# Optimization experiments

Hardware: AMD Instinct MI355X
Metric: run time of the kernel (lower is better)

Reference implementation:

```python
import jax, jax.numpy as jnp
import numpy as np
import math

D_MODEL = 768
N_HEAD = 12
HEAD_DIM = D_MODEL // N_HEAD
B = 4
W = 32
HW = W * W


def setup_inputs() -> dict:
    key = jax.random.key(0)
    k1, k2, k3 = jax.random.split(key, 3)
    x = jax.random.normal(k1, (B, HW, D_MODEL), dtype=jnp.float32)
    w_qkv = jax.random.normal(k2, (3 * D_MODEL, D_MODEL), dtype=jnp.float32) * (D_MODEL ** -0.5)
    w_out = jax.random.normal(k3, (D_MODEL, D_MODEL), dtype=jnp.float32) * (D_MODEL ** -0.5)
    gamma = jnp.ones((D_MODEL,), dtype=jnp.float32)
    return {"x": x, "w_qkv": w_qkv, "w_out": w_out, "gamma": gamma}


def _axial_sincos(w, head_dim, dtype):
    # Axial RoPE: first half of head_dim encodes row position, second half column.
    dim_half = head_dim // 2
    inv_freq = 1.0 / (10000.0 ** (jnp.arange(0, dim_half, 2, dtype=dtype) / dim_half))  # (dim_half//2,)
    pos = jnp.arange(w, dtype=dtype)
    ang = pos[:, None] * inv_freq[None, :]                 # (w, f)
    row = jnp.repeat(ang[:, None, :], w, axis=1)           # (w, w, f)
    col = jnp.repeat(ang[None, :, :], w, axis=0)           # (w, w, f)
    theta = jnp.concatenate([row, col], axis=-1).reshape(w * w, dim_half)  # (hw, head_dim//2)
    theta = jnp.concatenate([theta, theta], axis=-1)       # rotate-half layout -> (hw, head_dim)
    return jnp.sin(theta), jnp.cos(theta)


def _rotate_half(t):
    t1, t2 = jnp.split(t, 2, axis=-1)
    return jnp.concatenate([-t2, t1], axis=-1)


def _apply_rotary(t, sin, cos):
    return t * cos + _rotate_half(t) * sin


def _rms_norm(x, gamma, eps=1e-6):
    return x * jax.lax.rsqrt(jnp.mean(x * x, axis=-1, keepdims=True) + eps) * gamma


def _attn_mask(w):
    # Faithful to the torch source: mask[center, neighbor] = False, else True.
    # torch SDPA bool semantics: True = attend. So 3x3 neighbors are EXCLUDED.
    idx = jnp.arange(w * w)
    r, c = idx // w, idx % w
    neighbor = (jnp.abs(r[:, None] - r[None, :]) <= 1) & (jnp.abs(c[:, None] - c[None, :]) <= 1)
    return ~neighbor  # (hw, hw) bool, True = allowed


def reference(x, w_qkv, w_out, gamma):
    Bx, hw, d = x.shape
    w = int(math.isqrt(hw))
    h, hd = N_HEAD, HEAD_DIM
    sin, cos = _axial_sincos(w, hd, x.dtype)               # (hw, hd) each
    xn = _rms_norm(x, gamma)
    qkv = xn @ w_qkv.T                                     # (B, hw, 3d)
    qkv = qkv.reshape(Bx, hw, 3, h, hd)
    q = jnp.transpose(qkv[:, :, 0], (0, 2, 1, 3))          # (B, h, hw, hd)
    k = jnp.transpose(qkv[:, :, 1], (0, 2, 1, 3))
    v = jnp.transpose(qkv[:, :, 2], (0, 2, 1, 3))
    q = _apply_rotary(q, sin, cos)
    k = _apply_rotary(k, sin, cos)
    allow = _attn_mask(w)
    scale = 1.0 / jnp.sqrt(jnp.asarray(hd, x.dtype))
    scores = jnp.einsum('bhid,bhjd->bhij', q, k) * scale   # (B, h, hw, hw)
    scores = jnp.where(allow[None, None], scores, jnp.asarray(-jnp.inf, x.dtype))
    probs = jax.nn.softmax(scores, axis=-1)
    out = jnp.einsum('bhij,bhjd->bhid', probs, v)          # (B, h, hw, hd)
    out = jnp.transpose(out, (0, 2, 1, 3)).reshape(Bx, hw, d)
    return out @ w_out.T
```

## Files before the change

kernel.cpp:

```cpp
#include <hip/hip_runtime.h>

typedef __attribute__((ext_vector_type(8))) short short8;
typedef __attribute__((ext_vector_type(4))) float f32x4;
typedef __attribute__((ext_vector_type(4))) unsigned short ushort4_t;
typedef unsigned short ushort_t;
typedef unsigned long long u64;

#define D_MODEL 768
#define NHEAD 12
#define HD 64
#define BATCH 4
#define HWIDTH 32
#define HW 1024
#define TOK (BATCH*HW)
#define QKV_N (3*D_MODEL)
#define BH (BATCH*NHEAD)
#define QSCALE 0.18033688f

__device__ __forceinline__ ushort_t f2bf(float f) {
    union { float f; unsigned u; } v; v.f = f;
    unsigned u = v.u;
    unsigned r = u + 0x7FFFu + ((u >> 16) & 1u);
    return (ushort_t)(r >> 16);
}
__device__ __forceinline__ float ex2(float x) {
    float r; asm("v_exp_f32 %0, %1" : "=v"(r) : "v"(x)); return r;
}
__device__ __forceinline__ unsigned cvtpk(float lo, float hi) {
    unsigned r; asm("v_cvt_pk_bf16_f32 %0, %1, %2" : "=v"(r) : "v"(lo), "v"(hi)); return r;
}

__global__ __launch_bounds__(256) void prep_kernel(const float* __restrict__ x,
                                                   const float* __restrict__ gamma,
                                                   ushort_t* __restrict__ xn,
                                                   const float* __restrict__ w_qkv,
                                                   ushort_t* __restrict__ wq,
                                                   const float* __restrict__ w_out,
                                                   ushort_t* __restrict__ wo,
                                                   float* __restrict__ sint,
                                                   float* __restrict__ cost) {
    int blk = blockIdx.x;
    if (blk < 1024) {
        int wave = threadIdx.x >> 6, lane = threadIdx.x & 63;
        int t = blk * 4 + wave;
        const float* xr = x + (size_t)t * D_MODEL;
        float v[12]; float ss = 0.f;
        #pragma unroll
        for (int j = 0; j < 12; ++j) { v[j] = xr[lane + j*64]; ss += v[j]*v[j]; }
        #pragma unroll
        for (int m = 1; m < 64; m <<= 1) ss += __shfl_xor(ss, m, 64);
        float r = rsqrtf(ss * (1.f/768.f) + 1e-6f);
        ushort_t* o = xn + (size_t)t * D_MODEL;
        #pragma unroll
        for (int j = 0; j < 12; ++j) o[lane + j*64] = f2bf(v[j] * r * gamma[lane + j*64]);
    } else if (blk < 2752) {
        int i = (blk - 1024) * 1024 + threadIdx.x * 4;
        float4 v = *(const float4*)&w_qkv[i];
        uint2 pk; pk.x = cvtpk(v.x, v.y); pk.y = cvtpk(v.z, v.w);
        *(uint2*)&wq[i] = pk;
    } else if (blk < 3328) {
        int i = (blk - 2752) * 1024 + threadIdx.x * 4;
        float4 v = *(const float4*)&w_out[i];
        uint2 pk; pk.x = cvtpk(v.x, v.y); pk.y = cvtpk(v.z, v.w);
        *(uint2*)&wo[i] = pk;
    } else {
        int i = (blk - 3328) * 256 + threadIdx.x;
        int p = i >> 5, j = i & 31;
        int r = p >> 5, c = p & 31;
        int jj = j & 15;
        float freq = powf(10000.f, -(float)(2*jj) / 32.f);
        float pos = (j < 16) ? (float)r : (float)c;
        float th = pos * freq;
        sint[i] = sinf(th);
        cost[i] = cosf(th);
    }
}

template<int NTILES, int EPI>
__global__ __launch_bounds__(256, 2) void gemm128(const ushort_t* __restrict__ A,
                                                  const ushort_t* __restrict__ B,
                                                  const float* __restrict__ sint,
                                                  const float* __restrict__ cost,
                                                  ushort_t* __restrict__ Qr,
                                                  ushort_t* __restrict__ Kr,
                                                  ushort_t* __restrict__ VTt,
                                                  float* __restrict__ C) {
    __shared__ ushort_t As[2][128*64];
    __shared__ ushort_t Bs[2][128*64];
    const int K = 768;
    constexpr int NR = NTILES / 2;
    int c = blockIdx.x & 7;
    int l = blockIdx.x >> 3;
    int mtile = (c >> 1)*8 + l / NR;
    int ntile = (c & 1)*NR + l % NR;
    int tm = mtile * 128, tn = ntile * 128;
    int w = threadIdx.x >> 6, lane = threadIdx.x & 63;
    int wr = w >> 1, wc = w & 1;
    int l15 = lane & 15, l4 = lane >> 4;

    const ushort_t* mat = (w < 2) ? A : B;
    int mbase = (w < 2) ? tm : tn;
    ushort_t* lds_half = (w < 2) ? &As[0][0] : &Bs[0][0];
    int r0w = (w & 1) * 64;
    int srow = r0w + (lane >> 3);
    int sslot = (lane & 7) ^ (srow & 7);
    const ushort_t* gsrc0 = mat + (size_t)(mbase + srow)*K + sslot*8;

    auto stage = [&](int buf, int kstep) {
        int k0 = kstep * 64;
        #pragma unroll
        for (int j = 0; j < 8; ++j) {
            const ushort_t* g = gsrc0 + (size_t)(j*8)*K + k0;
            __builtin_amdgcn_global_load_lds((const __attribute__((address_space(1))) void*)g,
                (__attribute__((address_space(3))) void*)(lds_half + (size_t)buf*8192 + (r0w + j*8)*64),
                16, 0, 0);
        }
    };

    f32x4 acc[4][4] = {};
    auto compute = [&](int bi) {
        short8 af[4][2], bfx[4][2];
        #pragma unroll
        for (int mi = 0; mi < 4; ++mi) {
            int row = wr*64 + mi*16 + l15;
            #pragma unroll
            for (int kk = 0; kk < 2; ++kk)
                af[mi][kk] = *(const short8*)&As[bi][row*64 + ((kk*4 + l4) ^ (row & 7))*8];
        }
        #pragma unroll
        for (int ni = 0; ni < 4; ++ni) {
            int row = wc*64 + ni*16 + l15;
            #pragma unroll
            for (int kk = 0; kk < 2; ++kk)
                bfx[ni][kk] = *(const short8*)&Bs[bi][row*64 + ((kk*4 + l4) ^ (row & 7))*8];
        }
        #pragma unroll
        for (int kk = 0; kk < 2; ++kk)
            #pragma unroll
            for (int mi = 0; mi < 4; ++mi)
                #pragma unroll
                for (int ni = 0; ni < 4; ++ni)
                    acc[mi][ni] = __builtin_amdgcn_mfma_f32_16x16x32_bf16(af[mi][kk], bfx[ni][kk], acc[mi][ni], 0, 0, 0);
    };

    stage(0, 0);
    for (int t = 0; t < 12; ++t) {
        asm volatile("s_waitcnt vmcnt(0)" ::: "memory");
        __builtin_amdgcn_s_barrier();
        if (t < 11) stage((t + 1) & 1, t + 1);
        compute(t & 1);
    }

    if constexpr (EPI == 0) {
        int col_base = tn + wc*64;
        int region = col_base / 768;
        int h = (col_base % 768) >> 6;
        if (region < 2) {
            ushort_t* dst = (region == 0) ? Qr : Kr;
            float scale = (region == 0) ? QSCALE : 1.f;
            #pragma unroll
            for (int mi = 0; mi < 4; ++mi) {
                #pragma unroll
                for (int ni = 0; ni < 2; ++ni) {
                    int d = ni*16 + l15;
                    #pragma unroll
                    for (int r = 0; r < 4; ++r) {
                        int pt = tm + wr*64 + mi*16 + l4*4 + r;
                        int b = pt >> 10, p = pt & 1023;
                        float s = sint[p*32 + d], cc = cost[p*32 + d];
                        float t0 = acc[mi][ni][r], t1 = acc[mi][ni+2][r];
                        size_t o = (size_t)(b*NHEAD + h)*HW*HD + (size_t)p*HD + d;
                        dst[o]      = f2bf((t0*cc - t1*s) * scale);
                        dst[o + 32] = f2bf((t1*cc + t0*s) * scale);
                    }
                }
            }
        } else {
            #pragma unroll
            for (int mi = 0; mi < 4; ++mi) {
                int pt = tm + wr*64 + mi*16 + l4*4;
                int b = pt >> 10, p = pt & 1023;
                size_t hb = (size_t)(b*NHEAD + h)*HD*HW;
                #pragma unroll
                for (int ni = 0; ni < 4; ++ni) {
                    int d = ni*16 + l15;
                    ushort4_t pk;
                    pk.x = f2bf(acc[mi][ni][0]);
                    pk.y = f2bf(acc[mi][ni][1]);
                    pk.z = f2bf(acc[mi][ni][2]);
                    pk.w = f2bf(acc[mi][ni][3]);
                    *(ushort4_t*)&VTt[hb + (size_t)d*HW + p] = pk;
                }
            }
        }
    } else {
        #pragma unroll
        for (int mi = 0; mi < 4; ++mi)
            #pragma unroll
            for (int ni = 0; ni < 4; ++ni)
                #pragma unroll
                for (int r = 0; r < 4; ++r) {
                    int row = tm + wr*64 + mi*16 + l4*4 + r;
                    int col = tn + wc*64 + ni*16 + l15;
                    C[(size_t)row*(128*NTILES) + col] = acc[mi][ni][r];
                }
    }
}

__global__ __launch_bounds__(256, 3) void attn_kernel(const ushort_t* __restrict__ Q,
                                                      const ushort_t* __restrict__ Kt,
                                                      const ushort_t* __restrict__ VT,
                                                      ushort_t* __restrict__ Ao) {
    __shared__ ushort_t Kb[2][64*64];
    __shared__ ushort_t Vb[2][64*64];
    __shared__ ushort_t P[4][16][72];
    int flat = blockIdx.x;
    int swz = (flat & 7) * 96 + (flat >> 3);
    int bh = swz >> 4;
    int qtile = swz & 15;
    int w = threadIdx.x >> 6, lane = threadIdx.x & 63;
    int l15 = lane & 15, l4 = lane >> 4;
    int qbase = qtile * 64 + w * 16;
    int q = qbase + l15;
    int qr = q >> 5, qc = q & 31;
    const ushort_t* Qh = Q + (size_t)bh * HW * HD;
    const ushort_t* Kh = Kt + (size_t)bh * HW * HD;
    const ushort_t* Vh = VT + (size_t)bh * HD * HW;
    short8 aq0 = *(const short8*)&Qh[(size_t)q*64 + l4*8];
    short8 aq1 = *(const short8*)&Qh[(size_t)q*64 + 32 + l4*8];
    unsigned pat = (qc == 0) ? 3u : (7u << (qc - 1));
    float m = -1e30f, lsum = 0.f;
    f32x4 oacc[4] = {};

    auto stage = [&](int bufi, int kv) {
        #pragma unroll
        for (int is = 0; is < 2; ++is) {
            int c = is*256 + w*64 + lane;
            int row = c >> 3;
            int col16 = (c & 7) ^ (row & 7);
            const ushort_t* ga = Kh + (size_t)(kv + row)*64 + col16*8;
            __builtin_amdgcn_global_load_lds((const __attribute__((address_space(1))) void*)ga,
                (__attribute__((address_space(3))) void*)(&Kb[bufi][(size_t)(is*256 + w*64)*8]), 16, 0, 0);
            const ushort_t* gv = Vh + (size_t)row*HW + kv + col16*8;
            __builtin_amdgcn_global_load_lds((const __attribute__((address_space(1))) void*)gv,
                (__attribute__((address_space(3))) void*)(&Vb[bufi][(size_t)(is*256 + w*64)*8]), 16, 0, 0);
        }
    };

    stage(0, 0);

    for (int t = 0; t < 16; ++t) {
        asm volatile("s_waitcnt vmcnt(0)" ::: "memory");
        __builtin_amdgcn_s_barrier();
        if (t < 15) stage((t + 1) & 1, (t + 1) * 64);
        int cur = t & 1;
        int kv = t * 64;
        int sw = l15 & 7;
        f32x4 s[4];
        __builtin_amdgcn_s_setprio(1);
        #pragma unroll
        for (int st = 0; st < 4; ++st) {
            int krow = st*16 + l15;
            short8 bk0 = *(const short8*)&Kb[cur][(size_t)krow*64 + (size_t)((l4 ^ sw))*8];
            short8 bk1 = *(const short8*)&Kb[cur][(size_t)krow*64 + (size_t)(((4+l4) ^ sw))*8];
            f32x4 z = {};
            z = __builtin_amdgcn_mfma_f32_16x16x32_bf16(bk0, aq0, z, 0, 0, 0);
            z = __builtin_amdgcn_mfma_f32_16x16x32_bf16(bk1, aq1, z, 0, 0, 0);
            s[st] = z;
        }
        __builtin_amdgcn_s_setprio(0);
        short8 va0[4], va1[4];
        #pragma unroll
        for (int dt = 0; dt < 4; ++dt) {
            int vrow = dt*16 + l15;
            va0[dt] = *(const short8*)&Vb[cur][(size_t)vrow*64 + (size_t)((l4 ^ sw))*8];
            va1[dt] = *(const short8*)&Vb[cur][(size_t)vrow*64 + (size_t)(((4+l4) ^ sw))*8];
        }
        int dr = qr - (kv >> 5);
        if (dr >= -1 && dr <= 2) {
            u64 tm = 0;
            if (dr <= 1) tm |= (u64)pat;
            if (dr >= 0) tm |= ((u64)pat) << 32;
            u64 sub = tm >> (l4*4);
            #pragma unroll
            for (int st = 0; st < 4; ++st)
                #pragma unroll
                for (int i = 0; i < 4; ++i)
                    if ((sub >> (st*16 + i)) & 1) s[st][i] = -1e30f;
        }
        float vmax = fmaxf(
            fmaxf(fmaxf(fmaxf(s[0][0], s[0][1]), fmaxf(s[0][2], s[0][3])),
                  fmaxf(fmaxf(s[1][0], s[1][1]), fmaxf(s[1][2], s[1][3]))),
            fmaxf(fmaxf(fmaxf(s[2][0], s[2][1]), fmaxf(s[2][2], s[2][3])),
                  fmaxf(fmaxf(s[3][0], s[3][1]), fmaxf(s[3][2], s[3][3]))));
        vmax = fmaxf(vmax, __shfl_xor(vmax, 16, 64));
        vmax = fmaxf(vmax, __shfl_xor(vmax, 32, 64));
        if (__any(vmax - m > 8.f)) {
            float mn = fmaxf(m, vmax);
            float sf = ex2(m - mn);
            lsum *= sf;
            #pragma unroll
            for (int dt = 0; dt < 4; ++dt)
                #pragma unroll
                for (int i = 0; i < 4; ++i) oacc[dt][i] *= sf;
            m = mn;
        }
        float ls = 0.f;
        #pragma unroll
        for (int st = 0; st < 4; ++st) {
            float p0 = ex2(s[st][0] - m), p1 = ex2(s[st][1] - m);
            float p2 = ex2(s[st][2] - m), p3 = ex2(s[st][3] - m);
            ls += (p0 + p1) + (p2 + p3);
            uint2 pk;
            pk.x = cvtpk(p0, p1);
            pk.y = cvtpk(p2, p3);
            *(uint2*)&P[w][l15][st*16 + l4*4] = pk;
        }
        ls += __shfl_xor(ls, 16, 64);
        ls += __shfl_xor(ls, 32, 64);
        lsum += ls;
        short8 pf0 = *(const short8*)&P[w][l15][l4*8];
        short8 pf1 = *(const short8*)&P[w][l15][32 + l4*8];
        __builtin_amdgcn_s_setprio(1);
        #pragma unroll
        for (int dt = 0; dt < 4; ++dt) {
            oacc[dt] = __builtin_amdgcn_mfma_f32_16x16x32_bf16(va0[dt], pf0, oacc[dt], 0, 0, 0);
            oacc[dt] = __builtin_amdgcn_mfma_f32_16x16x32_bf16(va1[dt], pf1, oacc[dt], 0, 0, 0);
        }
        __builtin_amdgcn_s_setprio(0);
    }
    int b = bh / NHEAD, h = bh % NHEAD;
    float rl = 1.f / lsum;
    size_t obase = ((size_t)b*HW + q)*D_MODEL + h*64;
    #pragma unroll
    for (int dt = 0; dt < 4; ++dt) {
        uint2 pk;
        pk.x = cvtpk(oacc[dt][0]*rl, oacc[dt][1]*rl);
        pk.y = cvtpk(oacc[dt][2]*rl, oacc[dt][3]*rl);
        *(uint2*)&Ao[obase + dt*16 + l4*4] = pk;
    }
}

extern "C" void kernel_launch(void* const* d_in, const int* in_sizes, int n_in,
                              void* d_out, int out_size, void* d_ws, size_t ws_size,
                              hipStream_t stream) {
    const float* x      = (const float*)d_in[0];
    const float* w_qkv  = (const float*)d_in[1];
    const float* w_out  = (const float*)d_in[2];
    const float* gamma  = (const float*)d_in[3];
    float* out = (float*)d_out;

    char* ws = (char*)d_ws;
    size_t off = 0;
    auto alloc = [&](size_t bytes) { char* p = ws + off; off += (bytes + 255) & ~255ull; return p; };
    ushort_t* xn   = (ushort_t*)alloc((size_t)TOK*D_MODEL*2);
    ushort_t* wq   = (ushort_t*)alloc((size_t)QKV_N*D_MODEL*2);
    ushort_t* wo   = (ushort_t*)alloc((size_t)D_MODEL*D_MODEL*2);
    float* sint    = (float*)alloc((size_t)HW*32*4);
    float* cost    = (float*)alloc((size_t)HW*32*4);
    ushort_t* Qr   = (ushort_t*)alloc((size_t)BH*HW*HD*2);
    ushort_t* Kr   = (ushort_t*)alloc((size_t)BH*HW*HD*2);
    ushort_t* VTt  = (ushort_t*)alloc((size_t)BH*HD*HW*2);
    ushort_t* Ao   = (ushort_t*)alloc((size_t)TOK*D_MODEL*2);

    prep_kernel<<<3456, 256, 0, stream>>>(x, gamma, xn, w_qkv, wq, w_out, wo, sint, cost);
    gemm128<18,0><<<576, 256, 0, stream>>>(xn, wq, sint, cost, Qr, Kr, VTt, nullptr);
    attn_kernel<<<768, 256, 0, stream>>>(Qr, Kr, VTt, Ao);
    gemm128<6,1><<<192, 256, 0, stream>>>(Ao, wo, nullptr, nullptr, nullptr, nullptr, nullptr, out);
}
```

Before: 72.80 us.

## Software-pipeline attention loop to compute next tile's QK scores during softmax

Restructures the flash-attention KV loop into a ping-pong schedule. The next tile's QK^T MFMAs and V fragment loads are issued before the current tile's PV MFMAs, and the global-to-LDS stage now prefetches two tiles ahead. The aim is to overlap softmax VALU work and LDS latency with matrix-core work. The cost is roughly double the register state for scores and V fragments, which could lower occupancy or cause spills.

```diff
diff --git a/kernel.cpp b/kernel.cpp
--- a/kernel.cpp
+++ b/kernel.cpp
@@ -229,6 +229,7 @@
     short8 aq0 = *(const short8*)&Qh[(size_t)q*64 + l4*8];
     short8 aq1 = *(const short8*)&Qh[(size_t)q*64 + 32 + l4*8];
     unsigned pat = (qc == 0) ? 3u : (7u << (qc - 1));
+    int sw = l15 & 7;
     float m = -1e30f, lsum = 0.f;
     f32x4 oacc[4] = {};
 
@@ -247,35 +248,32 @@
         }
     };
 
-    stage(0, 0);
-
-    for (int t = 0; t < 16; ++t) {
-        asm volatile("s_waitcnt vmcnt(0)" ::: "memory");
-        __builtin_amdgcn_s_barrier();
-        if (t < 15) stage((t + 1) & 1, (t + 1) * 64);
-        int cur = t & 1;
-        int kv = t * 64;
-        int sw = l15 & 7;
-        f32x4 s[4];
+    auto ldK = [&](int buf, f32x4 (&s)[4]) {
         __builtin_amdgcn_s_setprio(1);
         #pragma unroll
         for (int st = 0; st < 4; ++st) {
             int krow = st*16 + l15;
-            short8 bk0 = *(const short8*)&Kb[cur][(size_t)krow*64 + (size_t)((l4 ^ sw))*8];
-            short8 bk1 = *(const short8*)&Kb[cur][(size_t)krow*64 + (size_t)(((4+l4) ^ sw))*8];
+            short8 bk0 = *(const short8*)&Kb[buf][(size_t)krow*64 + (size_t)((l4 ^ sw))*8];
+            short8 bk1 = *(const short8*)&Kb[buf][(size_t)krow*64 + (size_t)(((4+l4) ^ sw))*8];
             f32x4 z = {};
             z = __builtin_amdgcn_mfma_f32_16x16x32_bf16(bk0, aq0, z, 0, 0, 0);
             z = __builtin_amdgcn_mfma_f32_16x16x32_bf16(bk1, aq1, z, 0, 0, 0);
             s[st] = z;
         }
         __builtin_amdgcn_s_setprio(0);
-        short8 va0[4], va1[4];
+    };
+    auto ldV = [&](int buf, short8 (&va0)[4], short8 (&va1)[4]) {
         #pragma unroll
         for (int dt = 0; dt < 4; ++dt) {
             int vrow = dt*16 + l15;
-            va0[dt] = *(const short8*)&Vb[cur][(size_t)vrow*64 + (size_t)((l4 ^ sw))*8];
-            va1[dt] = *(const short8*)&Vb[cur][(size_t)vrow*64 + (size_t)(((4+l4) ^ sw))*8];
-        }
+            va0[dt] = *(const short8*)&Vb[buf][(size_t)vrow*64 + (size_t)((l4 ^ sw))*8];
+            va1[dt] = *(const short8*)&Vb[buf][(size_t)vrow*64 + (size_t)(((4+l4) ^ sw))*8];
+        }
+    };
+
+    auto tile_step = [&](f32x4 (&s)[4], short8 (&va0)[4], short8 (&va1)[4],
+                         f32x4 (&sn)[4], short8 (&vn0)[4], short8 (&vn1)[4], int t) {
+        int kv = t * 64;
         int dr = qr - (kv >> 5);
         if (dr >= -1 && dr <= 2) {
             u64 tm = 0;
@@ -321,6 +319,13 @@
         lsum += ls;
         short8 pf0 = *(const short8*)&P[w][l15][l4*8];
         short8 pf1 = *(const short8*)&P[w][l15][32 + l4*8];
+        if (t < 15) {
+            asm volatile("s_waitcnt vmcnt(0) lgkmcnt(0)" ::: "memory");
+            __builtin_amdgcn_s_barrier();
+            if (t < 14) stage(t & 1, (t + 2) * 64);
+            ldK((t + 1) & 1, sn);
+            ldV((t + 1) & 1, vn0, vn1);
+        }
         __builtin_amdgcn_s_setprio(1);
         #pragma unroll
         for (int dt = 0; dt < 4; ++dt) {
@@ -328,7 +333,22 @@
             oacc[dt] = __builtin_amdgcn_mfma_f32_16x16x32_bf16(va1[dt], pf1, oacc[dt], 0, 0, 0);
         }
         __builtin_amdgcn_s_setprio(0);
-    }
+    };
+
+    stage(0, 0);
+    asm volatile("s_waitcnt vmcnt(0)" ::: "memory");
+    __builtin_amdgcn_s_barrier();
+    stage(1, 64);
+    f32x4 sA[4], sB[4];
+    short8 vA0[4], vA1[4], vB0[4], vB1[4];
+    ldK(0, sA);
+    ldV(0, vA0, vA1);
+
+    for (int it = 0; it < 8; ++it) {
+        tile_step(sA, vA0, vA1, sB, vB0, vB1, 2*it);
+        tile_step(sB, vB0, vB1, sA, vA0, vA1, 2*it + 1);
+    }
+
     int b = bh / NHEAD, h = bh % NHEAD;
     float rl = 1.f / lsum;
     size_t obase = ((size_t)b*HW + q)*D_MODEL + h*64;
```

New measurement: 78.14 us. +7.3%, slower.
